# Performance work log

Hardware: AMD Instinct MI355X
Metric: run time of the kernel (lower is better)

## Reference

```python
import jax, jax.numpy as jnp
import numpy as np

TOPK = 2
ROUTE_SCALE = 1.0


def setup_inputs() -> dict:
    key = jax.random.key(0)
    ks = jax.random.split(key, 9)
    B, T, C, E, H = 4, 2048, 1024, 8, 2752
    s = 0.02  # init scale for weights
    return {
        "x": jax.random.normal(ks[0], (B, T, C), dtype=jnp.float32),
        "gate_w": jax.random.normal(ks[1], (E, C), dtype=jnp.float32) * s,
        "expert_bias": jnp.zeros((E,), dtype=jnp.float32),
        "w1": jax.random.normal(ks[2], (E, C, H), dtype=jnp.float32) * s,
        "w2": jax.random.normal(ks[3], (E, H, C), dtype=jnp.float32) * s,
        "w3": jax.random.normal(ks[4], (E, C, H), dtype=jnp.float32) * s,
        "sw1": jax.random.normal(ks[5], (C, H), dtype=jnp.float32) * s,
        "sw2": jax.random.normal(ks[6], (H, C), dtype=jnp.float32) * s,
        "sw3": jax.random.normal(ks[7], (C, H), dtype=jnp.float32) * s,
    }


def reference(x, gate_w, expert_bias, w1, w2, w3, sw1, sw2, sw3):
    B, T, C = x.shape
    E = gate_w.shape[0]
    xf = x.reshape(-1, C)  # (N, C)
    N = xf.shape[0]

    # --- ExpertGate (sigmoid scoring, aux-loss-free, eval mode) ---
    scores = jax.nn.sigmoid(xf @ gate_w.T)            # (N, E), original scores
    routing = scores + expert_bias[None, :]           # bias only affects selection
    _, idx = jax.lax.top_k(routing, TOPK)             # (N, TOPK)
    w = jnp.take_along_axis(scores, idx, axis=1)      # gather original scores
    w = w / (w.sum(axis=-1, keepdims=True) + 1e-8)    # sigmoid normalization
    w = w * ROUTE_SCALE

    # Scatter top-k weights into a dense (N, E) combine matrix
    gates = jnp.zeros((N, E), dtype=xf.dtype)
    gates = gates.at[jnp.arange(N)[:, None], idx].add(w)

    # --- Routed SwiGLU experts (dense compute, gated combine) ---
    y = jnp.zeros_like(xf)
    for e in range(E):  # small fixed loop over experts
        h = jax.nn.silu(xf @ w1[e]) * (xf @ w3[e])    # (N, H)
        y = y + gates[:, e:e + 1] * (h @ w2[e])

    # --- Shared expert (always on) ---
    y = y + (jax.nn.silu(xf @ sw1) * (xf @ sw3)) @ sw2

    return y.reshape(B, T, C)
```

## Files before the change

### kernel.cpp

```cpp
#include <hip/hip_runtime.h>
#include <hip/hip_bf16.h>
#include <stdint.h>

#define E_ 8
#define C_ 1024
#define H_ 2752
#define NTOK 8192
#define CAP_ROWS 17408

typedef unsigned short u16;
typedef __attribute__((ext_vector_type(8))) short bf16x8;
typedef __attribute__((ext_vector_type(4))) float f32x4;

static constexpr size_t SZ_XB    = (size_t)NTOK * C_ * 2;
static constexpr size_t SZ_WT    = (size_t)E_ * H_ * C_ * 2;
static constexpr size_t SZ_SWT   = (size_t)H_ * C_ * 2;
static constexpr size_t SZ_H     = (size_t)CAP_ROWS * H_ * 2;

static constexpr size_t OFF_XB   = 0;
static constexpr size_t OFF_W1T  = OFF_XB   + SZ_XB;
static constexpr size_t OFF_W3T  = OFF_W1T  + SZ_WT;
static constexpr size_t OFF_W2T  = OFF_W3T  + SZ_WT;
static constexpr size_t OFF_SW1T = OFF_W2T  + SZ_WT;
static constexpr size_t OFF_SW3T = OFF_SW1T + SZ_SWT;
static constexpr size_t OFF_SW2T = OFF_SW3T + SZ_SWT;
static constexpr size_t OFF_H    = OFF_SW2T + SZ_SWT;
static constexpr size_t OFF_RIDX = OFF_H    + SZ_H;
static constexpr size_t OFF_RW   = OFF_RIDX + (size_t)NTOK*2*4;
static constexpr size_t OFF_OFFS = OFF_RW   + (size_t)NTOK*2*4;
static constexpr size_t OFF_PTOK = OFF_OFFS + 64;
static constexpr size_t OFF_PW   = OFF_PTOK + (size_t)CAP_ROWS*4;
static constexpr size_t WS_NEED  = OFF_PW   + (size_t)CAP_ROWS*4;

__device__ __forceinline__ u16 f2bf(float f) {
  union { float f; uint32_t u; } v; v.f = f;
  uint32_t r = v.u + 0x7FFFu + ((v.u >> 16) & 1u);
  return (u16)(r >> 16);
}

__device__ __forceinline__ void gld16(const void* g, const void* l) {
  uint32_t lo = (uint32_t)(uintptr_t)l;
  lo = __builtin_amdgcn_readfirstlane(lo);
  __builtin_amdgcn_global_load_lds(
      (const __attribute__((address_space(1))) void*)g,
      (__attribute__((address_space(3))) void*)(uintptr_t)lo, 16, 0, 0);
}

#define MFMA16(A,B,C) __builtin_amdgcn_mfma_f32_16x16x32_bf16((A),(B),(C),0,0,0)

__global__ __launch_bounds__(256) void gate_kernel(
    const float* __restrict__ x, const float* __restrict__ gw,
    const float* __restrict__ bias, u16* __restrict__ xb,
    int* __restrict__ ridx, float* __restrict__ rw)
{
  const int n = blockIdx.x, t = threadIdx.x;
  const float4 v = *(const float4*)(x + (size_t)n * C_ + t * 4);
  union { u16 u[4]; uint2 d; } pk;
  pk.u[0] = f2bf(v.x); pk.u[1] = f2bf(v.y); pk.u[2] = f2bf(v.z); pk.u[3] = f2bf(v.w);
  *(uint2*)(xb + (size_t)n * C_ + t * 4) = pk.d;

  float p[E_];
#pragma unroll
  for (int e = 0; e < E_; ++e) {
    const float4 g = *(const float4*)(gw + (size_t)e * C_ + t * 4);
    p[e] = v.x * g.x + v.y * g.y + v.z * g.z + v.w * g.w;
  }
#pragma unroll
  for (int e = 0; e < E_; ++e)
    for (int off = 32; off > 0; off >>= 1) p[e] += __shfl_down(p[e], off);

  __shared__ float red[4][E_];
  const int wv = t >> 6;
  if ((t & 63) == 0) {
#pragma unroll
    for (int e = 0; e < E_; ++e) red[wv][e] = p[e];
  }
  __syncthreads();
  if (t == 0) {
    float sc[E_], rt[E_];
#pragma unroll
    for (int e = 0; e < E_; ++e) {
      const float d = red[0][e] + red[1][e] + red[2][e] + red[3][e];
      const float s = 1.f / (1.f + expf(-d));
      sc[e] = s; rt[e] = s + bias[e];
    }
    int i0 = 0; float b0 = rt[0];
#pragma unroll
    for (int e = 1; e < E_; ++e) if (rt[e] > b0) { b0 = rt[e]; i0 = e; }
    int i1 = -1; float b1 = -1e30f;
#pragma unroll
    for (int e = 0; e < E_; ++e) if (e != i0 && rt[e] > b1) { b1 = rt[e]; i1 = e; }
    const float s0 = sc[i0], s1 = sc[i1];
    const float inv = 1.f / (s0 + s1 + 1e-8f);
    ridx[2 * n] = i0; ridx[2 * n + 1] = i1;
    rw[2 * n] = s0 * inv; rw[2 * n + 1] = s1 * inv;
  }
}

__global__ __launch_bounds__(256) void transpose_cs_kernel(
    const float* __restrict__ w1, const float* __restrict__ w3,
    const float* __restrict__ sw1, const float* __restrict__ sw3,
    u16* __restrict__ w1t, u16* __restrict__ w3t,
    u16* __restrict__ sw1t, u16* __restrict__ sw3t)
{
  const int z = blockIdx.z;
  const float* src; u16* dst;
  if      (z < 8)  { src = w1 + (size_t)z * C_ * H_;       dst = w1t + (size_t)z * H_ * C_; }
  else if (z < 16) { src = w3 + (size_t)(z - 8) * C_ * H_; dst = w3t + (size_t)(z - 8) * H_ * C_; }
  else if (z == 16){ src = sw1; dst = sw1t; }
  else             { src = sw3; dst = sw3t; }
  __shared__ float tile[32][33];
  const int tx = threadIdx.x, ty = threadIdx.y;
  const int s0 = blockIdx.x * 32;
  const int r0 = blockIdx.y * 32;
#pragma unroll
  for (int i = 0; i < 4; ++i)
    tile[ty + 8 * i][tx] = src[(size_t)(r0 + ty + 8 * i) * H_ + s0 + tx];
  __syncthreads();
#pragma unroll
  for (int i = 0; i < 4; ++i)
    dst[(size_t)(s0 + ty + 8 * i) * C_ + r0 + tx] = f2bf(tile[tx][ty + 8 * i]);
}

__global__ __launch_bounds__(256) void transpose_sc_kernel(
    const float* __restrict__ w2, const float* __restrict__ sw2,
    u16* __restrict__ w2t, u16* __restrict__ sw2t)
{
  const int z = blockIdx.z;
  const float* src; u16* dst;
  if (z < 8) { src = w2 + (size_t)z * H_ * C_; dst = w2t + (size_t)z * C_ * H_; }
  else       { src = sw2; dst = sw2t; }
  __shared__ float tile[32][33];
  const int tx = threadIdx.x, ty = threadIdx.y;
  const int s0 = blockIdx.x * 32;
  const int r0 = blockIdx.y * 32;
#pragma unroll
  for (int i = 0; i < 4; ++i)
    tile[ty + 8 * i][tx] = src[(size_t)(r0 + ty + 8 * i) * C_ + s0 + tx];
  __syncthreads();
#pragma unroll
  for (int i = 0; i < 4; ++i)
    dst[(size_t)(s0 + ty + 8 * i) * H_ + r0 + tx] = f2bf(tile[tx][ty + 8 * i]);
}

__global__ __launch_bounds__(256) void route_scan_kernel(
    const int* __restrict__ ridx, const float* __restrict__ rw,
    int* __restrict__ offsets, int* __restrict__ perm_tok, float* __restrict__ perm_w)
{
  __shared__ int cnt[256][E_];
  __shared__ int pref[E_][257];
  __shared__ int offs[E_ + 1];
  __shared__ int totals[E_];
  const int t = threadIdx.x;
#pragma unroll
  for (int e = 0; e < E_; ++e) cnt[t][e] = 0;
  for (int j = 0; j < 64; ++j) { const int e = ridx[t * 64 + j]; cnt[t][e]++; }
  __syncthreads();
  if (t < E_) {
    int run = 0;
    for (int i = 0; i < 256; ++i) { pref[t][i] = run; run += cnt[i][t]; }
    totals[t] = run; pref[t][256] = run;
  }
  __syncthreads();
  if (t == 0) {
    int o = 0;
    for (int e = 0; e < E_; ++e) { offs[e] = o; o += (totals[e] + 127) & ~127; }
    offs[E_] = o;
    for (int i = 0; i <= E_; ++i) offsets[i] = offs[i];
  }
  __syncthreads();
#pragma unroll
  for (int e = 0; e < E_; ++e) cnt[t][e] = offs[e] + pref[e][t];
  for (int j = 0; j < 64; ++j) {
    const int a = t * 64 + j;
    const int e = ridx[a];
    const int p = cnt[t][e]++;
    perm_tok[p] = a >> 1;
    perm_w[p] = rw[a];
  }
  __syncthreads();
  for (int e = 0; e < E_; ++e) {
    for (int p = offs[e] + totals[e] + t; p < offs[e + 1]; p += 256) {
      perm_tok[p] = 0; perm_w[p] = 0.f;
    }
  }
}

template<int GATHER>
__global__ __launch_bounds__(256, 2) void gemm1_kernel(
    const u16* __restrict__ xb, const u16* __restrict__ w1t_all,
    const u16* __restrict__ w3t_all, u16* __restrict__ hout,
    const int* __restrict__ offsets, const int* __restrict__ perm_tok)
{
  __shared__ u16 lds[3 * 8192];
  const int t = threadIdx.x;
  const int row0 = blockIdx.x * 128;
  const int n0 = blockIdx.y * 128;
  int e = 0;
  if (GATHER) {
    if (row0 >= offsets[8]) return;
#pragma unroll
    for (int i = 0; i < 7; ++i) if (row0 >= offsets[i + 1]) e = i + 1;
  }
  const u16* w1t = GATHER ? (w1t_all + (size_t)e * (H_ * C_)) : w1t_all;
  const u16* w3t = GATHER ? (w3t_all + (size_t)e * (H_ * C_)) : w3t_all;

  const int tq = t >> 3;
  const int cb = (((t & 7) ^ (tq & 7)) << 4);
  const char* gA[4]; const char* gB1[4]; const char* gB3[4];
#pragma unroll
  for (int i = 0; i < 4; ++i) {
    const int m = i * 32 + tq;
    const int tok = GATHER ? perm_tok[row0 + m] : (row0 + m);
    gA[i]  = (const char*)xb  + (size_t)tok * (C_ * 2) + cb;
    const int nn = n0 + m;
    gB1[i] = (const char*)w1t + (size_t)nn * (C_ * 2) + cb;
    gB3[i] = (const char*)w3t + (size_t)nn * (C_ * 2) + cb;
  }
  char* lwave = (char*)lds + (t >> 6) * 1024;

  f32x4 acc1[4][4], acc3[4][4];
#pragma unroll
  for (int i = 0; i < 4; ++i)
#pragma unroll
    for (int j = 0; j < 4; ++j) { acc1[i][j] = f32x4{0.f,0.f,0.f,0.f}; acc3[i][j] = f32x4{0.f,0.f,0.f,0.f}; }

  const int lane = t & 63;
  const int l15 = lane & 15, lhi = lane >> 4, swz = lane & 7;
  const int wm = (t >> 7) & 1, wn = (t >> 6) & 1;
  int arow[4], brow[4];
#pragma unroll
  for (int f = 0; f < 4; ++f) {
    arow[f] = (wm * 64 + f * 16 + l15) * 128;
    brow[f] = (wn * 64 + f * 16 + l15) * 128;
  }
  const char* ldsc = (const char*)lds;

  for (int kt = 0; kt < C_ / 64; ++kt) {
    const int kb = kt * 128;
#pragma unroll
    for (int i = 0; i < 4; ++i) gld16(gA[i]  + kb, lwave + i * 4096);
#pragma unroll
    for (int i = 0; i < 4; ++i) gld16(gB1[i] + kb, lwave + 16384 + i * 4096);
#pragma unroll
    for (int i = 0; i < 4; ++i) gld16(gB3[i] + kb, lwave + 32768 + i * 4096);
    __syncthreads();
#pragma unroll
    for (int kk = 0; kk < 2; ++kk) {
      const int co = ((((kk << 2) | lhi)) ^ swz) << 4;
      bf16x8 a[4], b1[4], b3[4];
#pragma unroll
      for (int f = 0; f < 4; ++f) a[f]  = *(const bf16x8*)(ldsc + arow[f] + co);
#pragma unroll
      for (int f = 0; f < 4; ++f) b1[f] = *(const bf16x8*)(ldsc + 16384 + brow[f] + co);
#pragma unroll
      for (int f = 0; f < 4; ++f) b3[f] = *(const bf16x8*)(ldsc + 32768 + brow[f] + co);
#pragma unroll
      for (int mf = 0; mf < 4; ++mf)
#pragma unroll
        for (int nf = 0; nf < 4; ++nf) {
          acc1[mf][nf] = MFMA16(a[mf], b1[nf], acc1[mf][nf]);
          acc3[mf][nf] = MFMA16(a[mf], b3[nf], acc3[mf][nf]);
        }
    }
    __syncthreads();
  }

  const int rbase = row0 + wm * 64 + lhi * 4;
  const int cbase = n0 + wn * 64 + l15;
#pragma unroll
  for (int mf = 0; mf < 4; ++mf)
#pragma unroll
    for (int q = 0; q < 4; ++q) {
      const int r = rbase + mf * 16 + q;
      u16* hrow = hout + (size_t)r * H_;
#pragma unroll
      for (int nf = 0; nf < 4; ++nf) {
        const int c = cbase + nf * 16;
        if (c < H_) {
          const float v1 = acc1[mf][nf][q], v3 = acc3[mf][nf][q];
          const float sv = v1 / (1.f + __expf(-v1));
          hrow[c] = f2bf(sv * v3);
        }
      }
    }
}

template<int MODE>
__global__ __launch_bounds__(256, 2) void gemm2_kernel(
    const u16* __restrict__ hin, const u16* __restrict__ w2t_all,
    float* __restrict__ y, const int* __restrict__ offsets,
    const int* __restrict__ perm_tok, const float* __restrict__ perm_w)
{
  __shared__ u16 lds[2 * 8192];
  const int t = threadIdx.x;
  const int row0 = blockIdx.x * 128;
  const int n0 = blockIdx.y * 128;
  int e = 0;
  if (MODE == 1) {
    if (row0 >= offsets[8]) return;
#pragma unroll
    for (int i = 0; i < 7; ++i) if (row0 >= offsets[i + 1]) e = i + 1;
  }
  const u16* w2t = (MODE == 1) ? (w2t_all + (size_t)e * (C_ * H_)) : w2t_all;

  const int tq = t >> 3;
  const int cb = (((t & 7) ^ (tq & 7)) << 4);
  const char* gA[4]; const char* gB[4];
#pragma unroll
  for (int i = 0; i < 4; ++i) {
    gA[i] = (const char*)hin + (size_t)(row0 + i * 32 + tq) * (H_ * 2) + cb;
    gB[i] = (const char*)w2t + (size_t)(n0  + i * 32 + tq) * (H_ * 2) + cb;
  }
  char* lwave = (char*)lds + (t >> 6) * 1024;

  f32x4 acc[4][4];
#pragma unroll
  for (int i = 0; i < 4; ++i)
#pragma unroll
    for (int j = 0; j < 4; ++j) acc[i][j] = f32x4{0.f,0.f,0.f,0.f};

  const int lane = t & 63;
  const int l15 = lane & 15, lhi = lane >> 4, swz = lane & 7;
  const int wm = (t >> 7) & 1, wn = (t >> 6) & 1;
  int arow[4], brow[4];
#pragma unroll
  for (int f = 0; f < 4; ++f) {
    arow[f] = (wm * 64 + f * 16 + l15) * 128;
    brow[f] = (wn * 64 + f * 16 + l15) * 128;
  }
  const char* ldsc = (const char*)lds;

  for (int kt = 0; kt < H_ / 64; ++kt) {
    const int kb = kt * 128;
#pragma unroll
    for (int i = 0; i < 4; ++i) gld16(gA[i] + kb, lwave + i * 4096);
#pragma unroll
    for (int i = 0; i < 4; ++i) gld16(gB[i] + kb, lwave + 16384 + i * 4096);
    __syncthreads();
#pragma unroll
    for (int kk = 0; kk < 2; ++kk) {
      const int co = ((((kk << 2) | lhi)) ^ swz) << 4;
      bf16x8 a[4], b[4];
#pragma unroll
      for (int f = 0; f < 4; ++f) a[f] = *(const bf16x8*)(ldsc + arow[f] + co);
#pragma unroll
      for (int f = 0; f < 4; ++f) b[f] = *(const bf16x8*)(ldsc + 16384 + brow[f] + co);
#pragma unroll
      for (int mf = 0; mf < 4; ++mf)
#pragma unroll
        for (int nf = 0; nf < 4; ++nf)
          acc[mf][nf] = MFMA16(a[mf], b[nf], acc[mf][nf]);
    }
    __syncthreads();
  }

  const int rbase = row0 + wm * 64 + lhi * 4;
  const int cbase = n0 + wn * 64 + l15;
#pragma unroll
  for (int mf = 0; mf < 4; ++mf)
#pragma unroll
    for (int q = 0; q < 4; ++q) {
      const int r = rbase + mf * 16 + q;
      if (MODE == 0) {
        float* yr = y + (size_t)r * C_;
#pragma unroll
        for (int nf = 0; nf < 4; ++nf) yr[cbase + nf * 16] = acc[mf][nf][q];
      } else {
        const float wgt = perm_w[r];
        if (wgt != 0.f) {
          const int tok = perm_tok[r];
          float* yr = y + (size_t)tok * C_;
#pragma unroll
          for (int nf = 0; nf < 4; ++nf)
            atomicAdd(yr + cbase + nf * 16, wgt * acc[mf][nf][q]);
        }
      }
    }
}

extern "C" void kernel_launch(void* const* d_in, const int* in_sizes, int n_in,
                              void* d_out, int out_size, void* d_ws, size_t ws_size,
                              hipStream_t stream)
{
  const float* x    = (const float*)d_in[0];
  const float* gw   = (const float*)d_in[1];
  const float* bias = (const float*)d_in[2];
  const float* w1   = (const float*)d_in[3];
  const float* w2   = (const float*)d_in[4];
  const float* w3   = (const float*)d_in[5];
  const float* sw1  = (const float*)d_in[6];
  const float* sw2  = (const float*)d_in[7];
  const float* sw3  = (const float*)d_in[8];
  float* y = (float*)d_out;
  char* ws = (char*)d_ws;
  if (ws_size < WS_NEED) return;

  u16*   xb    = (u16*)(ws + OFF_XB);
  u16*   w1t   = (u16*)(ws + OFF_W1T);
  u16*   w3t   = (u16*)(ws + OFF_W3T);
  u16*   w2t   = (u16*)(ws + OFF_W2T);
  u16*   sw1t  = (u16*)(ws + OFF_SW1T);
  u16*   sw3t  = (u16*)(ws + OFF_SW3T);
  u16*   sw2t  = (u16*)(ws + OFF_SW2T);
  u16*   hbuf  = (u16*)(ws + OFF_H);
  int*   ridx  = (int*)(ws + OFF_RIDX);
  float* rwt   = (float*)(ws + OFF_RW);
  int*   offs  = (int*)(ws + OFF_OFFS);
  int*   ptok  = (int*)(ws + OFF_PTOK);
  float* pw    = (float*)(ws + OFF_PW);

  gate_kernel<<<NTOK, 256, 0, stream>>>(x, gw, bias, xb, ridx, rwt);
  transpose_cs_kernel<<<dim3(H_ / 32, C_ / 32, 18), dim3(32, 8), 0, stream>>>(
      w1, w3, sw1, sw3, w1t, w3t, sw1t, sw3t);
  transpose_sc_kernel<<<dim3(C_ / 32, H_ / 32, 9), dim3(32, 8), 0, stream>>>(
      w2, sw2, w2t, sw2t);
  route_scan_kernel<<<1, 256, 0, stream>>>(ridx, rwt, offs, ptok, pw);

  gemm1_kernel<0><<<dim3(NTOK / 128, 22), 256, 0, stream>>>(
      xb, sw1t, sw3t, hbuf, nullptr, nullptr);
  gemm2_kernel<0><<<dim3(NTOK / 128, 8), 256, 0, stream>>>(
      hbuf, sw2t, y, nullptr, nullptr, nullptr);
  gemm1_kernel<1><<<dim3(CAP_ROWS / 128, 22), 256, 0, stream>>>(
      xb, w1t, w3t, hbuf, offs, ptok);
  gemm2_kernel<1><<<dim3(CAP_ROWS / 128, 8), 256, 0, stream>>>(
      hbuf, w2t, y, offs, ptok, pw);
}
```

Before: 671.9 us.

## Merge shared and routed expert GEMMs into single launches per stage

Shared-expert and routed-expert GEMM1 and GEMM2 now run as one grid each, with block index choosing the weights and the row range in an enlarged hidden buffer. This cuts the four GEMM launches to two and lets shared and routed tiles fill the GPU together, avoiding tail underutilisation. The cost is that the shared expert output now goes through atomicAdd instead of plain stores, which needs an extra memset of y. GEMM1 weight-row indices are also clamped so the last partial N tile stays in bounds.

New measurement: 695.4 us. 3.5% more time.

```diff
diff --git a/kernel.cpp b/kernel.cpp
--- a/kernel.cpp
+++ b/kernel.cpp
@@ -7,6 +7,10 @@
 #define H_ 2752
 #define NTOK 8192
 #define CAP_ROWS 17408
+#define ROUTED_XB 136
+#define SHARED_XB 64
+#define SHARED_HBASE 17408
+#define HROWS 25600
 
 typedef unsigned short u16;
 typedef __attribute__((ext_vector_type(8))) short bf16x8;
@@ -15,7 +19,7 @@
 static constexpr size_t SZ_XB    = (size_t)NTOK * C_ * 2;
 static constexpr size_t SZ_WT    = (size_t)E_ * H_ * C_ * 2;
 static constexpr size_t SZ_SWT   = (size_t)H_ * C_ * 2;
-static constexpr size_t SZ_H     = (size_t)CAP_ROWS * H_ * 2;
+static constexpr size_t SZ_H     = (size_t)HROWS * H_ * 2;
 
 static constexpr size_t OFF_XB   = 0;
 static constexpr size_t OFF_W1T  = OFF_XB   + SZ_XB;
@@ -38,7 +42,7 @@
   return (u16)(r >> 16);
 }
 
-__device__ __forceinline__ void gld16(const void* g, const void* l) {
+__device__ __forceinline__ void gld16(const void* g, void* l) {
   uint32_t lo = (uint32_t)(uintptr_t)l;
   lo = __builtin_amdgcn_readfirstlane(lo);
   __builtin_amdgcn_global_load_lds(
@@ -186,24 +190,31 @@
   }
 }
 
-template<int GATHER>
-__global__ __launch_bounds__(256, 2) void gemm1_kernel(
+__global__ __launch_bounds__(256, 2) void gemm1_m(
     const u16* __restrict__ xb, const u16* __restrict__ w1t_all,
-    const u16* __restrict__ w3t_all, u16* __restrict__ hout,
-    const int* __restrict__ offsets, const int* __restrict__ perm_tok)
+    const u16* __restrict__ w3t_all, const u16* __restrict__ sw1t,
+    const u16* __restrict__ sw3t, u16* __restrict__ hbuf,
+    const int* __restrict__ offsets, const int* __restrict__ ptok)
 {
   __shared__ u16 lds[3 * 8192];
   const int t = threadIdx.x;
-  const int row0 = blockIdx.x * 128;
+  const int bx = blockIdx.x;
   const int n0 = blockIdx.y * 128;
-  int e = 0;
-  if (GATHER) {
+
+  const u16 *b1w, *b3w; int row0; size_t hr0; int gather;
+  if (bx < ROUTED_XB) {
+    row0 = bx * 128;
     if (row0 >= offsets[8]) return;
+    int e = 0;
 #pragma unroll
     for (int i = 0; i < 7; ++i) if (row0 >= offsets[i + 1]) e = i + 1;
-  }
-  const u16* w1t = GATHER ? (w1t_all + (size_t)e * (H_ * C_)) : w1t_all;
-  const u16* w3t = GATHER ? (w3t_all + (size_t)e * (H_ * C_)) : w3t_all;
+    b1w = w1t_all + (size_t)e * (H_ * C_);
+    b3w = w3t_all + (size_t)e * (H_ * C_);
+    hr0 = (size_t)row0; gather = 1;
+  } else {
+    row0 = (bx - ROUTED_XB) * 128;
+    b1w = sw1t; b3w = sw3t; hr0 = (size_t)SHARED_HBASE + row0; gather = 0;
+  }
 
   const int tq = t >> 3;
   const int cb = (((t & 7) ^ (tq & 7)) << 4);
@@ -211,11 +222,11 @@
 #pragma unroll
   for (int i = 0; i < 4; ++i) {
     const int m = i * 32 + tq;
-    const int tok = GATHER ? perm_tok[row0 + m] : (row0 + m);
-    gA[i]  = (const char*)xb  + (size_t)tok * (C_ * 2) + cb;
-    const int nn = n0 + m;
-    gB1[i] = (const char*)w1t + (size_t)nn * (C_ * 2) + cb;
-    gB3[i] = (const char*)w3t + (size_t)nn * (C_ * 2) + cb;
+    const int tok = gather ? ptok[row0 + m] : (row0 + m);
+    gA[i] = (const char*)xb + (size_t)tok * (C_ * 2) + cb;
+    int nn = n0 + m; if (nn > H_ - 1) nn = H_ - 1;
+    gB1[i] = (const char*)b1w + (size_t)nn * (C_ * 2) + cb;
+    gB3[i] = (const char*)b3w + (size_t)nn * (C_ * 2) + cb;
   }
   char* lwave = (char*)lds + (t >> 6) * 1024;
 
@@ -223,7 +234,7 @@
 #pragma unroll
   for (int i = 0; i < 4; ++i)
 #pragma unroll
-    for (int j = 0; j < 4; ++j) { acc1[i][j] = f32x4{0.f,0.f,0.f,0.f}; acc3[i][j] = f32x4{0.f,0.f,0.f,0.f}; }
+    for (int j = 0; j < 4; ++j) { acc1[i][j] = f32x4{0,0,0,0}; acc3[i][j] = f32x4{0,0,0,0}; }
 
   const int lane = t & 63;
   const int l15 = lane & 15, lhi = lane >> 4, swz = lane & 7;
@@ -266,14 +277,14 @@
     __syncthreads();
   }
 
-  const int rbase = row0 + wm * 64 + lhi * 4;
+  const int rbase = wm * 64 + lhi * 4;
   const int cbase = n0 + wn * 64 + l15;
 #pragma unroll
   for (int mf = 0; mf < 4; ++mf)
 #pragma unroll
     for (int q = 0; q < 4; ++q) {
       const int r = rbase + mf * 16 + q;
-      u16* hrow = hout + (size_t)r * H_;
+      u16* hrow = hbuf + (hr0 + r) * H_;
 #pragma unroll
       for (int nf = 0; nf < 4; ++nf) {
         const int c = cbase + nf * 16;
@@ -286,31 +297,39 @@
     }
 }
 
-template<int MODE>
-__global__ __launch_bounds__(256, 2) void gemm2_kernel(
-    const u16* __restrict__ hin, const u16* __restrict__ w2t_all,
-    float* __restrict__ y, const int* __restrict__ offsets,
-    const int* __restrict__ perm_tok, const float* __restrict__ perm_w)
+__global__ __launch_bounds__(256, 2) void gemm2_m(
+    const u16* __restrict__ hbuf, const u16* __restrict__ w2t_all,
+    const u16* __restrict__ sw2t, float* __restrict__ y,
+    const int* __restrict__ offsets, const int* __restrict__ ptok,
+    const float* __restrict__ pw)
 {
   __shared__ u16 lds[2 * 8192];
   const int t = threadIdx.x;
-  const int row0 = blockIdx.x * 128;
+  const int bx = blockIdx.x;
   const int n0 = blockIdx.y * 128;
-  int e = 0;
-  if (MODE == 1) {
+
+  int row0; size_t hr0; const u16* bW; int routed;
+  if (bx < ROUTED_XB) {
+    row0 = bx * 128;
     if (row0 >= offsets[8]) return;
+    int e = 0;
 #pragma unroll
     for (int i = 0; i < 7; ++i) if (row0 >= offsets[i + 1]) e = i + 1;
-  }
-  const u16* w2t = (MODE == 1) ? (w2t_all + (size_t)e * (C_ * H_)) : w2t_all;
+    bW = w2t_all + (size_t)e * (C_ * H_);
+    hr0 = (size_t)row0; routed = 1;
+  } else {
+    row0 = (bx - ROUTED_XB) * 128;
+    bW = sw2t; hr0 = (size_t)SHARED_HBASE + row0; routed = 0;
+  }
 
   const int tq = t >> 3;
   const int cb = (((t & 7) ^ (tq & 7)) << 4);
   const char* gA[4]; const char* gB[4];
 #pragma unroll
   for (int i = 0; i < 4; ++i) {
-    gA[i] = (const char*)hin + (size_t)(row0 + i * 32 + tq) * (H_ * 2) + cb;
-    gB[i] = (const char*)w2t + (size_t)(n0  + i * 32 + tq) * (H_ * 2) + cb;
+    const int m = i * 32 + tq;
+    gA[i] = (const char*)hbuf + (hr0 + m) * (size_t)(H_ * 2) + cb;
+    gB[i] = (const char*)bW + (size_t)(n0 + m) * (H_ * 2) + cb;
   }
   char* lwave = (char*)lds + (t >> 6) * 1024;
 
@@ -318,7 +337,7 @@
 #pragma unroll
   for (int i = 0; i < 4; ++i)
 #pragma unroll
-    for (int j = 0; j < 4; ++j) acc[i][j] = f32x4{0.f,0.f,0.f,0.f};
+    for (int j = 0; j < 4; ++j) acc[i][j] = f32x4{0,0,0,0};
 
   const int lane = t & 63;
   const int l15 = lane & 15, lhi = lane >> 4, swz = lane & 7;
@@ -331,7 +350,7 @@
   }
   const char* ldsc = (const char*)lds;
 
-  for (int kt = 0; kt < H_ / 64; ++kt) {
+  for (int kt = 0; kt < 43; ++kt) {
     const int kb = kt * 128;
 #pragma unroll
     for (int i = 0; i < 4; ++i) gld16(gA[i] + kb, lwave + i * 4096);
@@ -355,26 +374,20 @@
     __syncthreads();
   }
 
-  const int rbase = row0 + wm * 64 + lhi * 4;
+  const int rbase = wm * 64 + lhi * 4;
   const int cbase = n0 + wn * 64 + l15;
 #pragma unroll
   for (int mf = 0; mf < 4; ++mf)
 #pragma unroll
     for (int q = 0; q < 4; ++q) {
-      const int r = rbase + mf * 16 + q;
-      if (MODE == 0) {
-        float* yr = y + (size_t)r * C_;
-#pragma unroll
-        for (int nf = 0; nf < 4; ++nf) yr[cbase + nf * 16] = acc[mf][nf][q];
-      } else {
-        const float wgt = perm_w[r];
-        if (wgt != 0.f) {
-          const int tok = perm_tok[r];
-          float* yr = y + (size_t)tok * C_;
-#pragma unroll
-          for (int nf = 0; nf < 4; ++nf)
-            atomicAdd(yr + cbase + nf * 16, wgt * acc[mf][nf][q]);
-        }
+      const int hr = (int)hr0 + rbase + mf * 16 + q;
+      const float wgt = routed ? pw[hr] : 1.0f;
+      if (wgt != 0.f) {
+        const int tok = routed ? ptok[hr] : (hr - SHARED_HBASE);
+        float* yr = y + (size_t)tok * C_;
+#pragma unroll
+        for (int nf = 0; nf < 4; ++nf)
+          atomicAdd(yr + cbase + nf * 16, wgt * acc[mf][nf][q]);
       }
     }
 }
@@ -410,6 +423,7 @@
   int*   ptok  = (int*)(ws + OFF_PTOK);
   float* pw    = (float*)(ws + OFF_PW);
 
+  hipMemsetAsync(y, 0, (size_t)out_size * 4, stream);
   gate_kernel<<<NTOK, 256, 0, stream>>>(x, gw, bias, xb, ridx, rwt);
   transpose_cs_kernel<<<dim3(H_ / 32, C_ / 32, 18), dim3(32, 8), 0, stream>>>(
       w1, w3, sw1, sw3, w1t, w3t, sw1t, sw3t);
@@ -417,12 +431,8 @@
       w2, sw2, w2t, sw2t);
   route_scan_kernel<<<1, 256, 0, stream>>>(ridx, rwt, offs, ptok, pw);
 
-  gemm1_kernel<0><<<dim3(NTOK / 128, 22), 256, 0, stream>>>(
-      xb, sw1t, sw3t, hbuf, nullptr, nullptr);
-  gemm2_kernel<0><<<dim3(NTOK / 128, 8), 256, 0, stream>>>(
-      hbuf, sw2t, y, nullptr, nullptr, nullptr);
-  gemm1_kernel<1><<<dim3(CAP_ROWS / 128, 22), 256, 0, stream>>>(
-      xb, w1t, w3t, hbuf, offs, ptok);
-  gemm2_kernel<1><<<dim3(CAP_ROWS / 128, 8), 256, 0, stream>>>(
-      hbuf, w2t, y, offs, ptok, pw);
-}
+  gemm1_m<<<dim3(ROUTED_XB + SHARED_XB, 22), 256, 0, stream>>>(
+      xb, w1t, w3t, sw1t, sw3t, hbuf, offs, ptok);
+  gemm2_m<<<dim3(ROUTED_XB + SHARED_XB, 8), 256, 0, stream>>>(
+      hbuf, w2t, sw2t, y, offs, ptok, pw);
+}
```
